# Kernel tuning notes

Measured on AMD Instinct MI355X. Metric: run time of the kernel, lower is better.

Reference implementation:

```python
import jax, jax.numpy as jnp
import numpy as np


def setup_inputs() -> dict:
    key = jax.random.key(0)
    k1, k2 = jax.random.split(key)
    B, D, NUM_CLASSES = 8192, 128, 100
    features = jax.random.normal(k1, (B, D), dtype=jnp.float32)
    labels = jax.random.randint(k2, (B,), 0, NUM_CLASSES, dtype=jnp.int64)
    return {"features": features, "labels": labels}


def reference(features, labels):
    # temperature=0.07, clamp(min=0.01) -> 0.07
    TEMP = 0.07
    B = features.shape[0]
    dt = features.dtype

    # positive mask from labels: [B, B]
    mask = (labels[:, None] == labels[None, :]).astype(dt)

    # L2 normalize rows (F.normalize: x / max(||x||, eps))
    norm = jnp.sqrt(jnp.sum(features * features, axis=1, keepdims=True))
    f = features / jnp.maximum(norm, 1e-8)

    # similarity matrix, scaled and clamped to [-10, 10]
    sim = jnp.clip(jnp.matmul(f, f.T) / TEMP, -10.0, 10.0)

    eye = jnp.eye(B, dtype=dt)
    exp_sim = jnp.exp(sim)

    pos_sum = jnp.maximum(jnp.sum(exp_sim * (mask - eye), axis=1), 1e-8)
    neg_sum = jnp.maximum(jnp.sum(exp_sim * (1.0 - eye), axis=1), 1e-8)

    loss = -jnp.log(pos_sum / neg_sum)
    # NaN guard as in the original (returns 0 if any NaN)
    return jnp.where(jnp.any(jnp.isnan(loss)), jnp.zeros((), dt), jnp.mean(loss))
```

## Files before the change

kernel.cpp:

```cpp
#include <hip/hip_runtime.h>
#include <hip/hip_bf16.h>


using floatx4 = __attribute__((ext_vector_type(4))) float;
using intx4   = __attribute__((ext_vector_type(4))) int;
using intx8   = __attribute__((ext_vector_type(8))) int;
using llong2  = __attribute__((ext_vector_type(2))) long long;

constexpr int   Bn = 8192;
constexpr int   Dk = 128;
constexpr int   NSLICE = 32;
constexpr float PRESCALE = 4.5398160f;
constexpr float CLAMP    = 14.4269504f;
constexpr float LN2      = 0.69314718056f;
constexpr int   SCALE1   = 0x7F7F7F7F;

__global__ __launch_bounds__(256) void normalize_k(
    const float* __restrict__ feat, unsigned char* __restrict__ fb,
    float* __restrict__ out) {
  if (blockIdx.x == 0 && threadIdx.x == 0) *out = 0.f;
  const int row  = blockIdx.x * 4 + (threadIdx.x >> 6);
  const int lane = threadIdx.x & 63;
  const float2 v = ((const float2*)(feat + (size_t)row * Dk))[lane];
  float s = v.x * v.x + v.y * v.y;
#pragma unroll
  for (int m = 1; m < 64; m <<= 1) s += __shfl_xor(s, m);
  const float inv = PRESCALE / fmaxf(sqrtf(s), 1e-8f);
  const int packed = __builtin_amdgcn_cvt_pk_fp8_f32(v.x * inv, v.y * inv, 0, false);
  const int k0 = 2 * lane;
  const int p  = ((k0 & 31) >> 3) * 32 + (k0 >> 5) * 8 + (k0 & 7);
  *(unsigned short*)(fb + (size_t)row * Dk + p) = (unsigned short)(packed & 0xffff);
}

__global__ __launch_bounds__(256, 2) void simloss_k(
    const unsigned char* __restrict__ fb, const int* __restrict__ labels,
    float* __restrict__ rowpos2, float* __restrict__ rowneg2) {
  __shared__ __align__(16) unsigned char Bsh[256 * Dk];

  const int t     = threadIdx.x;
  const int lane  = t & 63;
  const int wave  = t >> 6;
  const int quad  = lane >> 4;
  const int lr    = lane & 15;
  const int jbase = blockIdx.x * 256;

  {
    const int chunk = t & 7;
    const int r0    = t >> 3;
#pragma unroll
    for (int it = 0; it < 8; ++it) {
      const int row = r0 + it * 32;
      const llong2 v = *(const llong2*)(fb + (size_t)(jbase + row) * Dk + chunk * 16);
      *(llong2*)(Bsh + row * Dk + ((chunk ^ (row & 7)) * 16)) = v;
    }
  }

  int labj16[8];
#pragma unroll
  for (int j = 0; j < 8; ++j) {
    const int l0 = labels[jbase + (2 * j) * 16 + lr];
    const int l1 = labels[jbase + (2 * j + 1) * 16 + lr];
    labj16[j] = l0 | (l1 << 16);
  }

  bool dl[4];
#pragma unroll
  for (int r = 0; r < 4; ++r) dl[r] = (quad * 4 + r) == lr;

  const int sw  = lr & 7;
  const int ch0 = ((quad * 2)     ^ sw) * 16;
  const int ch1 = ((quad * 2 + 1) ^ sw) * 16;

  __syncthreads();

#pragma unroll 1
  for (int p = 0; p < 2; ++p) {
    const int ibase = blockIdx.y * 256 + wave * 64 + p * 32;

    intx8 A0, A1;
    {
      const unsigned char* ap0 = fb + (size_t)(ibase + lr) * Dk + quad * 32;
      A0 = *(const intx8*)(ap0);
      A1 = *(const intx8*)(ap0 + 16 * Dk);
    }

    int li[2][4];
#pragma unroll
    for (int tt = 0; tt < 2; ++tt)
#pragma unroll
      for (int r = 0; r < 4; ++r)
        li[tt][r] = labels[ibase + tt * 16 + quad * 4 + r];

    float pos[2][4] = {};
    float neg[2][4] = {};

#pragma unroll
    for (int jt = 0; jt < 16; ++jt) {
      const unsigned char* bp = Bsh + (jt * 16 + lr) * Dk;
      const intx4 Blo = *(const intx4*)(bp + ch0);
      const intx4 Bhi = *(const intx4*)(bp + ch1);
      intx8 Bv;
      Bv[0] = Blo[0]; Bv[1] = Blo[1]; Bv[2] = Blo[2]; Bv[3] = Blo[3];
      Bv[4] = Bhi[0]; Bv[5] = Bhi[1]; Bv[6] = Bhi[2]; Bv[7] = Bhi[3];

      floatx4 acc0 = {0.f, 0.f, 0.f, 0.f};
      floatx4 acc1 = {0.f, 0.f, 0.f, 0.f};
      acc0 = __builtin_amdgcn_mfma_scale_f32_16x16x128_f8f6f4(
          A0, Bv, acc0, 0, 0, 0, SCALE1, 0, SCALE1);
      acc1 = __builtin_amdgcn_mfma_scale_f32_16x16x128_f8f6f4(
          A1, Bv, acc1, 0, 0, 0, SCALE1, 0, SCALE1);

      const int j0 = jbase + jt * 16;
      const int lj = (jt & 1) ? (labj16[jt >> 1] >> 16) : (labj16[jt >> 1] & 0xffff);
      float e0, e1, e2, e3;
      e0 = __builtin_amdgcn_exp2f(__builtin_amdgcn_fmed3f(acc0[0], -CLAMP, CLAMP));
      e1 = __builtin_amdgcn_exp2f(__builtin_amdgcn_fmed3f(acc0[1], -CLAMP, CLAMP));
      e2 = __builtin_amdgcn_exp2f(__builtin_amdgcn_fmed3f(acc0[2], -CLAMP, CLAMP));
      e3 = __builtin_amdgcn_exp2f(__builtin_amdgcn_fmed3f(acc0[3], -CLAMP, CLAMP));
      if (j0 == ibase) {
        if (dl[0]) e0 = 0.f;
        if (dl[1]) e1 = 0.f;
        if (dl[2]) e2 = 0.f;
        if (dl[3]) e3 = 0.f;
      }
      neg[0][0] += e0; neg[0][1] += e1; neg[0][2] += e2; neg[0][3] += e3;
      pos[0][0] += (li[0][0] == lj) ? e0 : 0.f;
      pos[0][1] += (li[0][1] == lj) ? e1 : 0.f;
      pos[0][2] += (li[0][2] == lj) ? e2 : 0.f;
      pos[0][3] += (li[0][3] == lj) ? e3 : 0.f;
      e0 = __builtin_amdgcn_exp2f(__builtin_amdgcn_fmed3f(acc1[0], -CLAMP, CLAMP));
      e1 = __builtin_amdgcn_exp2f(__builtin_amdgcn_fmed3f(acc1[1], -CLAMP, CLAMP));
      e2 = __builtin_amdgcn_exp2f(__builtin_amdgcn_fmed3f(acc1[2], -CLAMP, CLAMP));
      e3 = __builtin_amdgcn_exp2f(__builtin_amdgcn_fmed3f(acc1[3], -CLAMP, CLAMP));
      if (j0 == ibase + 16) {
        if (dl[0]) e0 = 0.f;
        if (dl[1]) e1 = 0.f;
        if (dl[2]) e2 = 0.f;
        if (dl[3]) e3 = 0.f;
      }
      neg[1][0] += e0; neg[1][1] += e1; neg[1][2] += e2; neg[1][3] += e3;
      pos[1][0] += (li[1][0] == lj) ? e0 : 0.f;
      pos[1][1] += (li[1][1] == lj) ? e1 : 0.f;
      pos[1][2] += (li[1][2] == lj) ? e2 : 0.f;
      pos[1][3] += (li[1][3] == lj) ? e3 : 0.f;
    }

#pragma unroll
    for (int tt = 0; tt < 2; ++tt)
#pragma unroll
      for (int r = 0; r < 4; ++r) {
        float p2 = pos[tt][r], n2 = neg[tt][r];
#pragma unroll
        for (int m = 1; m < 16; m <<= 1) {
          p2 += __shfl_xor(p2, m);
          n2 += __shfl_xor(n2, m);
        }
        if (lr == 0) {
          const int row = ibase + tt * 16 + quad * 4 + r;
          rowpos2[(size_t)blockIdx.x * Bn + row] = p2;
          rowneg2[(size_t)blockIdx.x * Bn + row] = n2;
        }
      }

    __builtin_amdgcn_sched_barrier(0);
  }
}

__global__ __launch_bounds__(256) void finalize_k(
    const float* __restrict__ rowpos2, const float* __restrict__ rowneg2,
    float* __restrict__ out) {
  const int row = blockIdx.x * 256 + threadIdx.x;
  float p = 0.f, n = 0.f;
#pragma unroll
  for (int s = 0; s < NSLICE; ++s) {
    p += rowpos2[(size_t)s * Bn + row];
    n += rowneg2[(size_t)s * Bn + row];
  }
  p = fmaxf(p, 1e-8f);
  n = fmaxf(n, 1e-8f);
  float loss = LN2 * (__builtin_amdgcn_logf(n) - __builtin_amdgcn_logf(p));
#pragma unroll
  for (int m = 1; m < 64; m <<= 1) loss += __shfl_xor(loss, m);
  __shared__ float partial[4];
  const int lane = threadIdx.x & 63, w = threadIdx.x >> 6;
  if (lane == 0) partial[w] = loss;
  __syncthreads();
  if (threadIdx.x == 0) {
    const float s = partial[0] + partial[1] + partial[2] + partial[3];
    atomicAdd(out, s * (1.0f / (float)Bn));
  }
}

extern "C" void kernel_launch(void* const* d_in, const int* in_sizes, int n_in,
                              void* d_out, int out_size, void* d_ws, size_t ws_size,
                              hipStream_t stream) {
  const float* feat   = (const float*)d_in[0];
  const int*   labels = (const int*)d_in[1];
  float* out = (float*)d_out;

  unsigned char* fb = (unsigned char*)d_ws;
  float* rowpos2 = (float*)((char*)d_ws + (size_t)Bn * Dk);
  float* rowneg2 = rowpos2 + (size_t)NSLICE * Bn;

  normalize_k<<<Bn / 4, 256, 0, stream>>>(feat, fb, out);
  dim3 grid(NSLICE, 32);
  simloss_k<<<grid, 256, 0, stream>>>(fb, labels, rowpos2, rowneg2);
  finalize_k<<<Bn / 256, 256, 0, stream>>>(rowpos2, rowneg2, out);
}
```

Before: 99.49 us.

## Fuse finalize into simloss via atomic row sums and last-block reduction

Replaces the per-slice partial row sums with atomicAdd into single per-row accumulators. The final log/mean reduction now runs in the last block to finish, detected with a global done counter, so the separate finalize kernel launch goes away. This removes one launch and the write and read of the 32-slice partial buffers, at the cost of atomic contention on each row (32 adders) and a serial tail where one block reduces all 8192 rows.

Measured after the change: 96.58 us. 2.9% less time.

```diff
diff --git a/kernel.cpp b/kernel.cpp
--- a/kernel.cpp
+++ b/kernel.cpp
@@ -10,6 +10,7 @@
 constexpr int   Bn = 8192;
 constexpr int   Dk = 128;
 constexpr int   NSLICE = 32;
+constexpr int   NBLK   = 32 * 32;
 constexpr float PRESCALE = 4.5398160f;
 constexpr float CLAMP    = 14.4269504f;
 constexpr float LN2      = 0.69314718056f;
@@ -17,8 +18,13 @@
 
 __global__ __launch_bounds__(256) void normalize_k(
     const float* __restrict__ feat, unsigned char* __restrict__ fb,
-    float* __restrict__ out) {
-  if (blockIdx.x == 0 && threadIdx.x == 0) *out = 0.f;
+    float* __restrict__ rowpos, float* __restrict__ rowneg,
+    unsigned int* __restrict__ done) {
+  if (blockIdx.x < 32) {
+    rowpos[blockIdx.x * 256 + threadIdx.x] = 0.f;
+    rowneg[blockIdx.x * 256 + threadIdx.x] = 0.f;
+  }
+  if (blockIdx.x == 32 && threadIdx.x == 0) *done = 0u;
   const int row  = blockIdx.x * 4 + (threadIdx.x >> 6);
   const int lane = threadIdx.x & 63;
   const float2 v = ((const float2*)(feat + (size_t)row * Dk))[lane];
@@ -34,7 +40,8 @@
 
 __global__ __launch_bounds__(256, 2) void simloss_k(
     const unsigned char* __restrict__ fb, const int* __restrict__ labels,
-    float* __restrict__ rowpos2, float* __restrict__ rowneg2) {
+    float* __restrict__ rowpos, float* __restrict__ rowneg,
+    unsigned int* __restrict__ done, float* __restrict__ out) {
   __shared__ __align__(16) unsigned char Bsh[256 * Dk];
 
   const int t     = threadIdx.x;
@@ -157,37 +164,39 @@
         }
         if (lr == 0) {
           const int row = ibase + tt * 16 + quad * 4 + r;
-          rowpos2[(size_t)blockIdx.x * Bn + row] = p2;
-          rowneg2[(size_t)blockIdx.x * Bn + row] = n2;
+          atomicAdd(&rowpos[row], p2);
+          atomicAdd(&rowneg[row], n2);
         }
       }
 
     __builtin_amdgcn_sched_barrier(0);
   }
-}
-
-__global__ __launch_bounds__(256) void finalize_k(
-    const float* __restrict__ rowpos2, const float* __restrict__ rowneg2,
-    float* __restrict__ out) {
-  const int row = blockIdx.x * 256 + threadIdx.x;
-  float p = 0.f, n = 0.f;
-#pragma unroll
-  for (int s = 0; s < NSLICE; ++s) {
-    p += rowpos2[(size_t)s * Bn + row];
-    n += rowneg2[(size_t)s * Bn + row];
-  }
-  p = fmaxf(p, 1e-8f);
-  n = fmaxf(n, 1e-8f);
-  float loss = LN2 * (__builtin_amdgcn_logf(n) - __builtin_amdgcn_logf(p));
-#pragma unroll
-  for (int m = 1; m < 64; m <<= 1) loss += __shfl_xor(loss, m);
-  __shared__ float partial[4];
-  const int lane = threadIdx.x & 63, w = threadIdx.x >> 6;
-  if (lane == 0) partial[w] = loss;
+
   __syncthreads();
-  if (threadIdx.x == 0) {
-    const float s = partial[0] + partial[1] + partial[2] + partial[3];
-    atomicAdd(out, s * (1.0f / (float)Bn));
+  int* flag = (int*)Bsh;
+  if (t == 0) {
+    __threadfence();
+    const unsigned int old = atomicAdd(done, 1u);
+    *flag = (old == (unsigned)(NBLK - 1)) ? 1 : 0;
+  }
+  __syncthreads();
+  if (*flag) {
+    __threadfence();
+    float acc = 0.f;
+#pragma unroll
+    for (int r = 0; r < Bn / 256; ++r) {
+      const int row = r * 256 + t;
+      const float pp = fmaxf(rowpos[row], 1e-8f);
+      const float nn = fmaxf(rowneg[row], 1e-8f);
+      acc += __builtin_amdgcn_logf(nn) - __builtin_amdgcn_logf(pp);
+    }
+#pragma unroll
+    for (int m = 1; m < 64; m <<= 1) acc += __shfl_xor(acc, m);
+    float* red = (float*)Bsh + 16;
+    if (lane == 0) red[wave] = acc;
+    __syncthreads();
+    if (t == 0)
+      *out = (red[0] + red[1] + red[2] + red[3]) * (LN2 / (float)Bn);
   }
 }
 
@@ -199,11 +208,11 @@
   float* out = (float*)d_out;
 
   unsigned char* fb = (unsigned char*)d_ws;
-  float* rowpos2 = (float*)((char*)d_ws + (size_t)Bn * Dk);
-  float* rowneg2 = rowpos2 + (size_t)NSLICE * Bn;
-
-  normalize_k<<<Bn / 4, 256, 0, stream>>>(feat, fb, out);
+  float* rowpos = (float*)((char*)d_ws + (size_t)Bn * Dk);
+  float* rowneg = rowpos + Bn;
+  unsigned int* done = (unsigned int*)(rowneg + Bn);
+
+  normalize_k<<<Bn / 4, 256, 0, stream>>>(feat, fb, rowpos, rowneg, done);
   dim3 grid(NSLICE, 32);
-  simloss_k<<<grid, 256, 0, stream>>>(fb, labels, rowpos2, rowneg2);
-  finalize_k<<<Bn / 256, 256, 0, stream>>>(rowpos2, rowneg2, out);
+  simloss_k<<<grid, 256, 0, stream>>>(fb, labels, rowpos, rowneg, done, out);
 }
```
